# Performance work log

Hardware: AMD Instinct MI355X
Metric: run time of the kernel (lower is better)

## Reference

```python
import jax, jax.numpy as jnp
import numpy as np

B, C, H, W = 8, 512, 96, 96
CQ = C // 4


def setup_inputs() -> dict:
    key = jax.random.key(0)
    ks = jax.random.split(key, 8)
    s = 1.0 / np.sqrt(C)
    return {
        "x": jax.random.normal(ks[0], (B, C, H, W), jnp.float32),
        "Wq": jax.random.normal(ks[1], (CQ, C), jnp.float32) * s,
        "bq": jax.random.normal(ks[2], (CQ,), jnp.float32) * 0.01,
        "Wk": jax.random.normal(ks[3], (CQ, C), jnp.float32) * s,
        "bk": jax.random.normal(ks[4], (CQ,), jnp.float32) * 0.01,
        "Wv": jax.random.normal(ks[5], (C, C), jnp.float32) * s,
        "bv": jax.random.normal(ks[6], (C,), jnp.float32) * 0.01,
        "gamma": jax.random.normal(ks[7], (1,), jnp.float32) * 0.1,
    }


def _conv1x1(x, Wt, b):
    # 1x1 conv == per-pixel channel matmul: [B,C,H,W] x [O,C] -> [B,O,H,W]
    return jnp.einsum("bchw,oc->bohw", x, Wt) + b[None, :, None, None]


def reference(x, Wq, bq, Wk, bk, Wv, bv, gamma):
    b, c, h, w = x.shape
    q = _conv1x1(x, Wq, bq)  # [B,CQ,H,W]
    k = _conv1x1(x, Wk, bk)  # [B,CQ,H,W]
    v = _conv1x1(x, Wv, bv)  # [B,C ,H,W]

    # column (height-axis) attention energies, diagonal masked to -inf
    energy_H = jnp.einsum("bchw,bcjw->bhwj", q, k)  # [B,H,W,H]
    diag = jnp.eye(h, dtype=bool)[:, None, :]  # [H,1,H] broadcast over W
    energy_H = jnp.where(diag[None], -jnp.inf, energy_H)
    # row (width-axis) attention energies
    energy_W = jnp.einsum("bchw,bchj->bhwj", q, k)  # [B,H,W,W]

    att = jax.nn.softmax(jnp.concatenate([energy_H, energy_W], axis=3), axis=3)
    att_H = att[..., :h]       # [B,H,W,H]
    att_W = att[..., h:h + w]  # [B,H,W,W]

    out_H = jnp.einsum("bcjw,bhwj->bchw", v, att_H)
    out_W = jnp.einsum("bchj,bhwj->bchw", v, att_W)
    return gamma[0] * (out_H + out_W) + x
```

## Files before the change

### kernel.cpp

```cpp
#include <hip/hip_runtime.h>


#define B_ 8
#define C_ 512
#define CQ_ 128
#define H_ 96
#define W_ 96
#define HW_ 9216
#define J_ 192

typedef __attribute__((ext_vector_type(8))) short short8;
typedef __attribute__((ext_vector_type(4))) float f32x4;

__device__ __forceinline__ unsigned short f2bf(float f) {
    unsigned u = __float_as_uint(f);
    u += 0x7FFFu + ((u >> 16) & 1u);
    return (unsigned short)(u >> 16);
}
__device__ __forceinline__ float bf2f(unsigned short h) {
    return __uint_as_float((unsigned)h << 16);
}
__device__ __forceinline__ unsigned short f2h(float f) {
    _Float16 h = (_Float16)f;
    return __builtin_bit_cast(unsigned short, h);
}
__device__ __forceinline__ float h2f(unsigned short u) {
    return (float)__builtin_bit_cast(_Float16, u);
}

__global__ __launch_bounds__(256) void k0_wconv(const float* __restrict__ Wq,
                                                const float* __restrict__ Wk,
                                                const float* __restrict__ Wv,
                                                unsigned short* __restrict__ Wqk,
                                                unsigned short* __restrict__ Wvb) {
    int i = blockIdx.x * 256 + threadIdx.x;
    if (i < 65536)        Wqk[i] = f2bf(Wq[i]);
    else if (i < 131072)  Wqk[i] = f2bf(Wk[i - 65536]);
    else                  Wvb[i - 131072] = f2bf(Wv[i - 131072]);
}

__global__ __launch_bounds__(256) void k1_xT(const float* __restrict__ x,
                                             unsigned short* __restrict__ xT) {
    __shared__ unsigned short t[32][33];
    int b = blockIdx.z, c0 = blockIdx.y * 32, p0 = blockIdx.x * 32;
    int tx = threadIdx.x, ty = threadIdx.y;
    const float* xb = x + (size_t)b * C_ * HW_;
    #pragma unroll
    for (int k = 0; k < 4; ++k) {
        int c = c0 + ty + k * 8;
        t[ty + k * 8][tx] = f2bf(xb[(size_t)c * HW_ + p0 + tx]);
    }
    __syncthreads();
    unsigned short* xTb = xT + (size_t)b * HW_ * C_;
    #pragma unroll
    for (int k = 0; k < 4; ++k) {
        int p = p0 + ty + k * 8;
        xTb[(size_t)p * C_ + c0 + tx] = t[tx][ty + k * 8];
    }
}

__global__ __launch_bounds__(512) void k2a_qk(const unsigned short* __restrict__ xT,
                                              const unsigned short* __restrict__ Wqk,
                                              const float* __restrict__ bq,
                                              const float* __restrict__ bk,
                                              unsigned short* __restrict__ Qb,
                                              unsigned short* __restrict__ Kb) {
    __shared__ alignas(16) unsigned short As[128][72];
    __shared__ alignas(16) unsigned short Bs[256][72];
    int t = threadIdx.x;
    int p0 = blockIdx.x * 128;
    int wid = t >> 6, lane = t & 63;
    int wr = wid >> 2, wc = wid & 3;
    const f32x4 zero = {0.f, 0.f, 0.f, 0.f};
    f32x4 acc[4][4];
    for (int m = 0; m < 4; ++m) for (int n = 0; n < 4; ++n) acc[m][n] = zero;
    for (int ks = 0; ks < 512; ks += 64) {
        #pragma unroll
        for (int s = 0; s < 2; ++s) {
            int q = t + s * 512; int row = q >> 3, c8 = (q & 7) << 3;
            *(uint4*)(&As[row][c8]) = *(const uint4*)(xT + ((size_t)(p0 + row) << 9) + ks + c8);
        }
        #pragma unroll
        for (int s = 0; s < 4; ++s) {
            int q = t + s * 512; int row = q >> 3, c8 = (q & 7) << 3;
            *(uint4*)(&Bs[row][c8]) = *(const uint4*)(Wqk + ((size_t)row << 9) + ks + c8);
        }
        __syncthreads();
        #pragma unroll
        for (int kk = 0; kk < 2; ++kk) {
            int ko = (kk << 5) + ((lane >> 4) << 3);
            short8 af[4], bfv[4];
            #pragma unroll
            for (int m = 0; m < 4; ++m) af[m] = *(const short8*)(&As[wr * 64 + m * 16 + (lane & 15)][ko]);
            #pragma unroll
            for (int n = 0; n < 4; ++n) bfv[n] = *(const short8*)(&Bs[wc * 64 + n * 16 + (lane & 15)][ko]);
            #pragma unroll
            for (int m = 0; m < 4; ++m)
                #pragma unroll
                for (int n = 0; n < 4; ++n)
                    acc[m][n] = __builtin_amdgcn_mfma_f32_16x16x32_bf16(af[m], bfv[n], acc[m][n], 0, 0, 0);
        }
        __syncthreads();
    }
    #pragma unroll
    for (int n = 0; n < 4; ++n) {
        int oc = wc * 64 + n * 16 + (lane & 15);
        float bias = (oc < 128) ? bq[oc] : bk[oc - 128];
        unsigned short* dst = (oc < 128) ? (Qb + oc) : (Kb + (oc - 128));
        #pragma unroll
        for (int m = 0; m < 4; ++m) {
            int pr = p0 + wr * 64 + m * 16 + ((lane >> 4) << 2);
            #pragma unroll
            for (int r = 0; r < 4; ++r)
                dst[(size_t)(pr + r) << 7] = f2bf(acc[m][n][r] + bias);
        }
    }
}

__global__ __launch_bounds__(512) void k2b_v(const unsigned short* __restrict__ xT,
                                             const unsigned short* __restrict__ Wvb,
                                             const float* __restrict__ bv,
                                             unsigned short* __restrict__ Vn) {
    __shared__ alignas(16) unsigned short As[256][72];
    __shared__ alignas(16) unsigned short Bs[128][72];
    int t = threadIdx.x;
    int oc0 = blockIdx.x * 256;
    int p0 = blockIdx.y * 128;
    int wid = t >> 6, lane = t & 63;
    int wr = wid >> 1, wc = wid & 1;
    const f32x4 zero = {0.f, 0.f, 0.f, 0.f};
    f32x4 acc[4][4];
    for (int m = 0; m < 4; ++m) for (int n = 0; n < 4; ++n) acc[m][n] = zero;
    for (int ks = 0; ks < 512; ks += 64) {
        #pragma unroll
        for (int s = 0; s < 4; ++s) {
            int q = t + s * 512; int row = q >> 3, c8 = (q & 7) << 3;
            *(uint4*)(&As[row][c8]) = *(const uint4*)(Wvb + ((size_t)(oc0 + row) << 9) + ks + c8);
        }
        #pragma unroll
        for (int s = 0; s < 2; ++s) {
            int q = t + s * 512; int row = q >> 3, c8 = (q & 7) << 3;
            *(uint4*)(&Bs[row][c8]) = *(const uint4*)(xT + ((size_t)(p0 + row) << 9) + ks + c8);
        }
        __syncthreads();
        #pragma unroll
        for (int kk = 0; kk < 2; ++kk) {
            int ko = (kk << 5) + ((lane >> 4) << 3);
            short8 af[4], bfv[4];
            #pragma unroll
            for (int m = 0; m < 4; ++m) af[m] = *(const short8*)(&As[wr * 64 + m * 16 + (lane & 15)][ko]);
            #pragma unroll
            for (int n = 0; n < 4; ++n) bfv[n] = *(const short8*)(&Bs[wc * 64 + n * 16 + (lane & 15)][ko]);
            #pragma unroll
            for (int m = 0; m < 4; ++m)
                #pragma unroll
                for (int n = 0; n < 4; ++n)
                    acc[m][n] = __builtin_amdgcn_mfma_f32_16x16x32_bf16(af[m], bfv[n], acc[m][n], 0, 0, 0);
        }
        __syncthreads();
    }
    int b = p0 / HW_;
    int hw0 = p0 - b * HW_;
    #pragma unroll
    for (int m = 0; m < 4; ++m) {
        int ocb = oc0 + wr * 64 + m * 16 + ((lane >> 4) << 2);
        #pragma unroll
        for (int n = 0; n < 4; ++n) {
            int hw = hw0 + wc * 64 + n * 16 + (lane & 15);
            #pragma unroll
            for (int r = 0; r < 4; ++r) {
                int oc = ocb + r;
                Vn[(size_t)(b * C_ + oc) * HW_ + hw] = f2bf(acc[m][n][r] + bv[oc]);
            }
        }
    }
}

__global__ __launch_bounds__(256) void k3_vt(const unsigned short* __restrict__ Vn,
                                             unsigned short* __restrict__ Vt) {
    __shared__ unsigned short tl[96][97];
    int plane = blockIdx.x;
    const unsigned short* src = Vn + (size_t)plane * HW_;
    unsigned short* dst = Vt + (size_t)plane * HW_;
    for (int e = threadIdx.x; e < HW_; e += 256) tl[e / 96][e % 96] = src[e];
    __syncthreads();
    for (int e = threadIdx.x; e < HW_; e += 256) { int w = e / 96, h = e % 96; dst[e] = tl[h][w]; }
}

__global__ __launch_bounds__(256) void k4_energy(const unsigned short* __restrict__ Qb,
                                                 const unsigned short* __restrict__ Kb,
                                                 unsigned short* __restrict__ att) {
    __shared__ alignas(16) unsigned short Qs[96][136];
    __shared__ alignas(16) unsigned short Ks[96][136];
    int t = threadIdx.x;
    int modeH = blockIdx.z;
    int b = blockIdx.y, v0 = blockIdx.x;
    size_t base, rstride, obase_off, ostride;
    if (!modeH) {
        base      = (size_t)((b * H_ + v0) * W_) * CQ_;
        rstride   = CQ_;
        obase_off = (size_t)((b * H_ + v0) * W_) * J_ + H_;
        ostride   = J_;
    } else {
        base      = ((size_t)(b * H_) * W_ + v0) * CQ_;
        rstride   = (size_t)W_ * CQ_;
        obase_off = ((size_t)(b * H_) * W_ + v0) * J_;
        ostride   = (size_t)W_ * J_;
    }
    for (int q = t; q < 1536; q += 256) {
        int row = q >> 4, c8 = (q & 15) << 3;
        *(uint4*)(&Qs[row][c8]) = *(const uint4*)(Qb + base + (size_t)row * rstride + c8);
        *(uint4*)(&Ks[row][c8]) = *(const uint4*)(Kb + base + (size_t)row * rstride + c8);
    }
    __syncthreads();
    int wid = t >> 6, lane = t & 63;
    int wr = wid >> 1, wc = wid & 1;
    const f32x4 zero = {0.f, 0.f, 0.f, 0.f};
    f32x4 acc[3][3];
    for (int m = 0; m < 3; ++m) for (int n = 0; n < 3; ++n) acc[m][n] = zero;
    #pragma unroll
    for (int ks = 0; ks < 128; ks += 32) {
        int ko = ks + ((lane >> 4) << 3);
        short8 af[3], bfv[3];
        #pragma unroll
        for (int m = 0; m < 3; ++m) af[m] = *(const short8*)(&Qs[wr * 48 + m * 16 + (lane & 15)][ko]);
        #pragma unroll
        for (int n = 0; n < 3; ++n) bfv[n] = *(const short8*)(&Ks[wc * 48 + n * 16 + (lane & 15)][ko]);
        #pragma unroll
        for (int m = 0; m < 3; ++m)
            #pragma unroll
            for (int n = 0; n < 3; ++n)
                acc[m][n] = __builtin_amdgcn_mfma_f32_16x16x32_bf16(af[m], bfv[n], acc[m][n], 0, 0, 0);
    }
    unsigned short* ob = att + obase_off;
    #pragma unroll
    for (int m = 0; m < 3; ++m) {
        int i = wr * 48 + m * 16 + ((lane >> 4) << 2);
        #pragma unroll
        for (int n = 0; n < 3; ++n) {
            int j = wc * 48 + n * 16 + (lane & 15);
            #pragma unroll
            for (int r = 0; r < 4; ++r) {
                float v = acc[m][n][r];
                if (modeH && (i + r) == j) v = -__builtin_inff();
                ob[(size_t)(i + r) * ostride + j] = f2h(v);
            }
        }
    }
}

__global__ __launch_bounds__(256) void k5_softmax(const unsigned short* __restrict__ att,
                                                  unsigned short* __restrict__ att2) {
    int r = blockIdx.x * 4 + (threadIdx.x >> 6);
    int lane = threadIdx.x & 63;
    const unsigned short* row = att + (size_t)r * J_;
    float e0 = h2f(row[lane]), e1 = h2f(row[lane + 64]), e2 = h2f(row[lane + 128]);
    float m = fmaxf(e0, fmaxf(e1, e2));
    #pragma unroll
    for (int off = 32; off; off >>= 1) m = fmaxf(m, __shfl_xor(m, off, 64));
    float p0 = __expf(e0 - m), p1 = __expf(e1 - m), p2 = __expf(e2 - m);
    float s = p0 + p1 + p2;
    #pragma unroll
    for (int off = 32; off; off >>= 1) s += __shfl_xor(s, off, 64);
    float inv = 1.f / s;
    unsigned short* orow = att2 + (size_t)r * J_;
    orow[lane]       = f2bf(p0 * inv);
    orow[lane + 64]  = f2bf(p1 * inv);
    orow[lane + 128] = f2bf(p2 * inv);
}

template <int MODE>
__global__ __launch_bounds__(256) void k67_agg(const unsigned short* __restrict__ Vsrc,
                                               const unsigned short* __restrict__ att2,
                                               unsigned short* __restrict__ dst) {
    __shared__ alignas(16) unsigned short As[128][104];
    __shared__ alignas(16) unsigned short Bs[96][104];
    int t = threadIdx.x;
    int c0 = blockIdx.x * 128;
    int b = blockIdx.y / 96;
    int v0 = blockIdx.y % 96;
    size_t abase, bbase, bstride;
    if (MODE == 0) {
        abase = (size_t)(b * C_ + c0) * HW_ + (size_t)v0 * W_;
        bbase = (size_t)((b * H_ + v0) * W_) * J_ + H_;
        bstride = J_;
    } else {
        abase = ((size_t)(b * C_ + c0) * W_ + v0) * H_;
        bbase = ((size_t)(b * H_) * W_ + v0) * J_;
        bstride = (size_t)W_ * J_;
    }
    {
        int row = t >> 1, cs = (t & 1) * 6;
        const unsigned short* src = Vsrc + abase + (size_t)row * HW_;
        #pragma unroll
        for (int i = 0; i < 6; ++i)
            *(uint4*)(&As[row][(cs + i) * 8]) = *(const uint4*)(src + (cs + i) * 8);
    }
    if (t < 192) {
        int row = t >> 1, cs = (t & 1) * 6;
        const unsigned short* src = att2 + bbase + (size_t)row * bstride;
        #pragma unroll
        for (int i = 0; i < 6; ++i)
            *(uint4*)(&Bs[row][(cs + i) * 8]) = *(const uint4*)(src + (cs + i) * 8);
    }
    __syncthreads();
    int wid = t >> 6, lane = t & 63;
    const f32x4 zero = {0.f, 0.f, 0.f, 0.f};
    f32x4 acc[2][6];
    for (int m = 0; m < 2; ++m) for (int n = 0; n < 6; ++n) acc[m][n] = zero;
    #pragma unroll
    for (int ks = 0; ks < 96; ks += 32) {
        int ko = ks + ((lane >> 4) << 3);
        short8 af[2], bfv[6];
        #pragma unroll
        for (int m = 0; m < 2; ++m) af[m] = *(const short8*)(&As[wid * 32 + m * 16 + (lane & 15)][ko]);
        #pragma unroll
        for (int n = 0; n < 6; ++n) bfv[n] = *(const short8*)(&Bs[n * 16 + (lane & 15)][ko]);
        #pragma unroll
        for (int m = 0; m < 2; ++m)
            #pragma unroll
            for (int n = 0; n < 6; ++n)
                acc[m][n] = __builtin_amdgcn_mfma_f32_16x16x32_bf16(af[m], bfv[n], acc[m][n], 0, 0, 0);
    }
    #pragma unroll
    for (int m = 0; m < 2; ++m) {
        int crel = wid * 32 + m * 16 + ((lane >> 4) << 2);
        #pragma unroll
        for (int n = 0; n < 6; ++n) {
            int col = n * 16 + (lane & 15);
            #pragma unroll
            for (int r = 0; r < 4; ++r)
                dst[abase + (size_t)(crel + r) * HW_ + col] = f2bf(acc[m][n][r]);
        }
    }
}

__global__ __launch_bounds__(256) void k8b_combine(const unsigned short* __restrict__ tmpW,
                                                   const unsigned short* __restrict__ tmpHT,
                                                   const float* __restrict__ x,
                                                   const float* __restrict__ gamma_p,
                                                   float* __restrict__ outp) {
    __shared__ unsigned tlp[96][49];
    int plane = blockIdx.x;
    int t = threadIdx.x;
    const unsigned short* src = tmpHT + (size_t)plane * HW_;
    for (int e = t; e < 1152; e += 256) {
        int w = e / 12, h8 = (e % 12) * 8;
        uint4 v = *(const uint4*)(src + w * 96 + h8);
        tlp[w][(h8 >> 1) + 0] = v.x;
        tlp[w][(h8 >> 1) + 1] = v.y;
        tlp[w][(h8 >> 1) + 2] = v.z;
        tlp[w][(h8 >> 1) + 3] = v.w;
    }
    __syncthreads();
    float g = gamma_p[0];
    const unsigned short* wp = tmpW + (size_t)plane * HW_;
    const float* xp = x + (size_t)plane * HW_;
    float* op = outp + (size_t)plane * HW_;
    #pragma unroll
    for (int i = 0; i < 9; ++i) {
        int m = t + 256 * i;
        int h = m / 24, w0 = (m % 24) * 4;
        int off = h * 96 + w0;
        f32x4 xv = *(const f32x4*)(xp + off);
        uint2 tw = *(const uint2*)(wp + off);
        unsigned short ws0 = (unsigned short)(tw.x & 0xFFFF);
        unsigned short ws1 = (unsigned short)(tw.x >> 16);
        unsigned short ws2 = (unsigned short)(tw.y & 0xFFFF);
        unsigned short ws3 = (unsigned short)(tw.y >> 16);
        f32x4 o;
        #pragma unroll
        for (int r = 0; r < 4; ++r) {
            unsigned u = tlp[w0 + r][h >> 1];
            unsigned short hv = (h & 1) ? (unsigned short)(u >> 16) : (unsigned short)(u & 0xFFFF);
            unsigned short wv = (r == 0) ? ws0 : (r == 1) ? ws1 : (r == 2) ? ws2 : ws3;
            o[r] = g * (bf2f(wv) + bf2f(hv)) + xv[r];
        }
        *(f32x4*)(op + off) = o;
    }
}

extern "C" void kernel_launch(void* const* d_in, const int* in_sizes, int n_in,
                              void* d_out, int out_size, void* d_ws, size_t ws_size,
                              hipStream_t stream) {
    const float* x  = (const float*)d_in[0];
    const float* Wq = (const float*)d_in[1];
    const float* bq = (const float*)d_in[2];
    const float* Wk = (const float*)d_in[3];
    const float* bk = (const float*)d_in[4];
    const float* Wv = (const float*)d_in[5];
    const float* bv = (const float*)d_in[6];
    const float* gm = (const float*)d_in[7];
    float* out = (float*)d_out;
    char* ws = (char*)d_ws;

    unsigned short* xT    = (unsigned short*)(ws + 0);
    unsigned short* attf  = (unsigned short*)(ws + 0);
    unsigned short* Vt    = (unsigned short*)(ws + 0);
    unsigned short* Vn    = (unsigned short*)(ws + 75497472);
    unsigned short* Qb    = (unsigned short*)(ws + 150994944);
    unsigned short* Kb    = (unsigned short*)(ws + 169869312);
    unsigned short* att2  = (unsigned short*)(ws + 150994944);
    unsigned short* Wqk   = (unsigned short*)(ws + 188743680);
    unsigned short* Wvb   = (unsigned short*)(ws + 189005824);

    k0_wconv<<<1536, 256, 0, stream>>>(Wq, Wk, Wv, Wqk, Wvb);
    k1_xT<<<dim3(288, 16, 8), dim3(32, 8, 1), 0, stream>>>(x, xT);
    k2a_qk<<<576, 512, 0, stream>>>(xT, Wqk, bq, bk, Qb, Kb);
    k2b_v<<<dim3(2, 576), 512, 0, stream>>>(xT, Wvb, bv, Vn);
    k4_energy<<<dim3(96, 8, 2), 256, 0, stream>>>(Qb, Kb, attf);
    k5_softmax<<<18432, 256, 0, stream>>>(attf, att2);
    k3_vt<<<4096, 256, 0, stream>>>(Vn, Vt);
    k67_agg<0><<<dim3(4, 768), 256, 0, stream>>>(Vn, att2, Vn);
    k67_agg<1><<<dim3(4, 768), 256, 0, stream>>>(Vt, att2, Vt);
    k8b_combine<<<4096, 256, 0, stream>>>(Vn, Vt, x, gm, out);
}
```

Baseline: 390.1 us.

## Use direct global-to-LDS loads in QK/V projection GEMMs and retile V GEMM

The QK and V projection GEMMs now stage their tiles with global_load_lds, which copies global memory straight into LDS without passing through registers. The padded LDS rows are removed to fit that layout, which may bring back bank conflicts on the MFMA fragment reads. The V GEMM is retiled so each block covers all 512 output channels for 64 pixels. xT is then read once per pixel tile instead of twice, while each block reloads the whole Wv matrix.

New measurement: 379.0 us. 1.03x faster.

```diff
diff --git a/kernel.cpp b/kernel.cpp
--- a/kernel.cpp
+++ b/kernel.cpp
@@ -26,6 +26,11 @@
 }
 __device__ __forceinline__ float h2f(unsigned short u) {
     return (float)__builtin_bit_cast(_Float16, u);
+}
+__device__ __forceinline__ void gl_lds16(const unsigned short* g, void* lds_base) {
+    __builtin_amdgcn_global_load_lds((const __attribute__((address_space(1))) void*)g,
+                                     (__attribute__((address_space(3))) void*)lds_base,
+                                     16, 0, 0);
 }
 
 __global__ __launch_bounds__(256) void k0_wconv(const float* __restrict__ Wq,
@@ -65,25 +70,26 @@
                                               const float* __restrict__ bk,
                                               unsigned short* __restrict__ Qb,
                                               unsigned short* __restrict__ Kb) {
-    __shared__ alignas(16) unsigned short As[128][72];
-    __shared__ alignas(16) unsigned short Bs[256][72];
+    __shared__ alignas(16) unsigned short As[128][64];
+    __shared__ alignas(16) unsigned short Bs[256][64];
     int t = threadIdx.x;
     int p0 = blockIdx.x * 128;
     int wid = t >> 6, lane = t & 63;
     int wr = wid >> 2, wc = wid & 3;
+    int srow = lane >> 3, sk8 = (lane & 7) << 3;
     const f32x4 zero = {0.f, 0.f, 0.f, 0.f};
     f32x4 acc[4][4];
     for (int m = 0; m < 4; ++m) for (int n = 0; n < 4; ++n) acc[m][n] = zero;
     for (int ks = 0; ks < 512; ks += 64) {
         #pragma unroll
-        for (int s = 0; s < 2; ++s) {
-            int q = t + s * 512; int row = q >> 3, c8 = (q & 7) << 3;
-            *(uint4*)(&As[row][c8]) = *(const uint4*)(xT + ((size_t)(p0 + row) << 9) + ks + c8);
-        }
-        #pragma unroll
-        for (int s = 0; s < 4; ++s) {
-            int q = t + s * 512; int row = q >> 3, c8 = (q & 7) << 3;
-            *(uint4*)(&Bs[row][c8]) = *(const uint4*)(Wqk + ((size_t)row << 9) + ks + c8);
+        for (int i = 0; i < 2; ++i) {
+            int q = wid * 2 + i; int row = q * 8 + srow;
+            gl_lds16(xT + ((size_t)(p0 + row) << 9) + ks + sk8, (char*)&As[0][0] + q * 1024);
+        }
+        #pragma unroll
+        for (int i = 0; i < 4; ++i) {
+            int q = wid * 4 + i; int row = q * 8 + srow;
+            gl_lds16(Wqk + ((size_t)row << 9) + ks + sk8, (char*)&Bs[0][0] + q * 1024);
         }
         __syncthreads();
         #pragma unroll
@@ -121,40 +127,39 @@
                                              const unsigned short* __restrict__ Wvb,
                                              const float* __restrict__ bv,
                                              unsigned short* __restrict__ Vn) {
-    __shared__ alignas(16) unsigned short As[256][72];
-    __shared__ alignas(16) unsigned short Bs[128][72];
+    __shared__ alignas(16) unsigned short As[512][64];
+    __shared__ alignas(16) unsigned short Bs[64][64];
     int t = threadIdx.x;
-    int oc0 = blockIdx.x * 256;
-    int p0 = blockIdx.y * 128;
+    int p0 = blockIdx.x * 64;
     int wid = t >> 6, lane = t & 63;
     int wr = wid >> 1, wc = wid & 1;
+    int srow = lane >> 3, sk8 = (lane & 7) << 3;
     const f32x4 zero = {0.f, 0.f, 0.f, 0.f};
-    f32x4 acc[4][4];
-    for (int m = 0; m < 4; ++m) for (int n = 0; n < 4; ++n) acc[m][n] = zero;
+    f32x4 acc[8][2];
+    for (int m = 0; m < 8; ++m) for (int n = 0; n < 2; ++n) acc[m][n] = zero;
     for (int ks = 0; ks < 512; ks += 64) {
         #pragma unroll
-        for (int s = 0; s < 4; ++s) {
-            int q = t + s * 512; int row = q >> 3, c8 = (q & 7) << 3;
-            *(uint4*)(&As[row][c8]) = *(const uint4*)(Wvb + ((size_t)(oc0 + row) << 9) + ks + c8);
-        }
-        #pragma unroll
-        for (int s = 0; s < 2; ++s) {
-            int q = t + s * 512; int row = q >> 3, c8 = (q & 7) << 3;
-            *(uint4*)(&Bs[row][c8]) = *(const uint4*)(xT + ((size_t)(p0 + row) << 9) + ks + c8);
+        for (int i = 0; i < 8; ++i) {
+            int q = wid * 8 + i; int row = q * 8 + srow;
+            gl_lds16(Wvb + ((size_t)row << 9) + ks + sk8, (char*)&As[0][0] + q * 1024);
+        }
+        {
+            int q = wid; int row = q * 8 + srow;
+            gl_lds16(xT + ((size_t)(p0 + row) << 9) + ks + sk8, (char*)&Bs[0][0] + q * 1024);
         }
         __syncthreads();
         #pragma unroll
         for (int kk = 0; kk < 2; ++kk) {
             int ko = (kk << 5) + ((lane >> 4) << 3);
-            short8 af[4], bfv[4];
-            #pragma unroll
-            for (int m = 0; m < 4; ++m) af[m] = *(const short8*)(&As[wr * 64 + m * 16 + (lane & 15)][ko]);
-            #pragma unroll
-            for (int n = 0; n < 4; ++n) bfv[n] = *(const short8*)(&Bs[wc * 64 + n * 16 + (lane & 15)][ko]);
-            #pragma unroll
-            for (int m = 0; m < 4; ++m)
+            short8 af[8], bfv[2];
+            #pragma unroll
+            for (int m = 0; m < 8; ++m) af[m] = *(const short8*)(&As[wr * 128 + m * 16 + (lane & 15)][ko]);
+            #pragma unroll
+            for (int n = 0; n < 2; ++n) bfv[n] = *(const short8*)(&Bs[wc * 32 + n * 16 + (lane & 15)][ko]);
+            #pragma unroll
+            for (int m = 0; m < 8; ++m)
                 #pragma unroll
-                for (int n = 0; n < 4; ++n)
+                for (int n = 0; n < 2; ++n)
                     acc[m][n] = __builtin_amdgcn_mfma_f32_16x16x32_bf16(af[m], bfv[n], acc[m][n], 0, 0, 0);
         }
         __syncthreads();
@@ -162,11 +167,11 @@
     int b = p0 / HW_;
     int hw0 = p0 - b * HW_;
     #pragma unroll
-    for (int m = 0; m < 4; ++m) {
-        int ocb = oc0 + wr * 64 + m * 16 + ((lane >> 4) << 2);
-        #pragma unroll
-        for (int n = 0; n < 4; ++n) {
-            int hw = hw0 + wc * 64 + n * 16 + (lane & 15);
+    for (int m = 0; m < 8; ++m) {
+        int ocb = wr * 128 + m * 16 + ((lane >> 4) << 2);
+        #pragma unroll
+        for (int n = 0; n < 2; ++n) {
+            int hw = hw0 + wc * 32 + n * 16 + (lane & 15);
             #pragma unroll
             for (int r = 0; r < 4; ++r) {
                 int oc = ocb + r;
@@ -407,7 +412,7 @@
     k0_wconv<<<1536, 256, 0, stream>>>(Wq, Wk, Wv, Wqk, Wvb);
     k1_xT<<<dim3(288, 16, 8), dim3(32, 8, 1), 0, stream>>>(x, xT);
     k2a_qk<<<576, 512, 0, stream>>>(xT, Wqk, bq, bk, Qb, Kb);
-    k2b_v<<<dim3(2, 576), 512, 0, stream>>>(xT, Wvb, bv, Vn);
+    k2b_v<<<1152, 512, 0, stream>>>(xT, Wvb, bv, Vn);
     k4_energy<<<dim3(96, 8, 2), 256, 0, stream>>>(Qb, Kb, attf);
     k5_softmax<<<18432, 256, 0, stream>>>(attf, att2);
     k3_vt<<<4096, 256, 0, stream>>>(Vn, Vt);
```
